# Optimization experiments

Measured on AMD Instinct MI355X. Metric: run time of the kernel, lower is better.

## Reference

```python
import jax, jax.numpy as jnp
import numpy as np

D_HID = 512
N_HEADS = 16
D_HEAD = D_HID // N_HEADS  # 32
D_FFN = 2048
B, N = 4, 1024
FACTOR = 0.5 / np.sqrt(D_HEAD)
EPS = 1e-5


def layer_norm(x, g, b):
    m = x.mean(-1, keepdims=True)
    v = ((x - m) ** 2).mean(-1, keepdims=True)
    return (x - m) / jnp.sqrt(v + EPS) * g + b


def setup_inputs() -> dict:
    key = jax.random.key(0)
    ks = jax.random.split(key, 24)
    s = 0.02
    p = lambda k, shape: jax.random.normal(k, shape, jnp.float32) * s
    inp = {
        'H': jax.random.normal(ks[0], (B, N, D_HID), jnp.float32),
        'V': jax.random.normal(ks[1], (B, N, 3, D_HID), jnp.float32),
        'D_batch': jax.random.normal(ks[2], (B, N, N), jnp.float32),
        'rbf_bias': jax.random.normal(ks[3], (B, 1, N, N), jnp.float32),
        'H_mask': jax.random.randint(ks[4], (B, N), 0, 2, jnp.int32),
        # attention sublayer params
        'g1': jnp.ones((D_HID,), jnp.float32), 'beta1': jnp.zeros((D_HID,), jnp.float32),
        'Wq': p(ks[5], (D_HID, 4 * D_HID)), 'bq': p(ks[6], (4 * D_HID,)),
        'Wk': p(ks[7], (D_HID, 4 * D_HID)), 'bk': p(ks[8], (4 * D_HID,)),
        'Wv': p(ks[9], (D_HID, D_HID)), 'bv': p(ks[10], (D_HID,)),
        'Wvv': p(ks[11], (D_HID, D_HID)),
        'Wo': p(ks[12], (D_HID, D_HID)), 'bo': p(ks[13], (D_HID,)),
        'Wvo': p(ks[14], (D_HID, D_HID)),
        # GVP FFN sublayer params
        'g2': jnp.ones((D_HID,), jnp.float32), 'beta2': jnp.zeros((D_HID,), jnp.float32),
        'Wlv': p(ks[15], (D_HID, 2 * D_HID)),
        'W1': p(ks[16], (2 * D_HID, D_FFN)), 'b1f': p(ks[17], (D_FFN,)),
        'W2': p(ks[18], (D_FFN, 2 * D_HID)), 'b2f': p(ks[19], (2 * D_HID,)),
    }
    return inp


def ept_forward(H, V, D_batch, rbf_bias, H_mask, g1, beta1, Wq, bq, Wk, bk, Wv, bv,
                Wvv, Wo, bo, Wvo, g2, beta2, Wlv, W1, b1f, W2, b2f):
    b, n, d = H.shape
    # ---- attention sublayer (pre-LN on H only, residual on H and V) ----
    Hn = layer_norm(H, g1, beta1)
    Hq = (Hn @ Wq + bq).reshape(b, n, N_HEADS, 4 * D_HEAD)
    Hk = (Hn @ Wk + bk).reshape(b, n, N_HEADS, 4 * D_HEAD)
    Hv = (Hn @ Wv + bv).reshape(b, n, N_HEADS, D_HEAD)
    # vector values: [b,n,3,d] -> [b,n,heads,3*dh]
    Vv = (V @ Wvv).reshape(b, n, 3, N_HEADS, D_HEAD).transpose(0, 1, 3, 2, 4)
    Vv = Vv.reshape(b, n, N_HEADS, 3 * D_HEAD)
    V_attn = jnp.concatenate([Hv, Vv], axis=-1)  # [b,n,h,4*dh]
    bias = rbf_bias + D_batch[:, None]  # [b,1,n,n]
    keep = (H_mask != 0)[:, None, None, :]  # mask keys
    bias = jnp.where(keep, bias, -jnp.inf)
    logits = jnp.einsum('bnhd,bmhd->bhnm', Hq, Hk) * FACTOR + bias
    attn = jax.nn.softmax(logits, axis=-1)
    res = jnp.einsum('bhnm,bmhd->bnhd', attn, V_attn)  # [b,n,h,4*dh]
    H_res = res[..., :D_HEAD].reshape(b, n, d)
    V_res = res[..., D_HEAD:].reshape(b, n, N_HEADS, 3, D_HEAD)
    V_res = V_res.transpose(0, 1, 3, 2, 4).reshape(b, n, 3, d)
    H = H + H_res @ Wo + bo
    V = V + V_res @ Wvo
    # ---- GVP FFN sublayer (pre-LN on H only, residual) ----
    Hn2 = layer_norm(H, g2, beta2)
    Vp = V @ Wlv  # [b,n,3,2d]
    V1, V2 = Vp[..., :d], Vp[..., d:]
    scaler = jnp.concatenate([Hn2, jnp.sqrt((V1 ** 2).sum(axis=-2))], axis=-1)
    h = jax.nn.silu(scaler @ W1 + b1f) @ W2 + b2f  # [b,n,2d]
    H = H + h[..., :d]
    V = V + h[..., None, d:] * V2
    return H, V


def reference(H, V, D_batch, rbf_bias, H_mask, g1, beta1, Wq, bq, Wk, bk, Wv, bv,
              Wvv, Wo, bo, Wvo, g2, beta2, Wlv, W1, b1f, W2, b2f):
    return ept_forward(H, V, D_batch, rbf_bias, H_mask, g1, beta1, Wq, bq, Wk, bk,
                       Wv, bv, Wvv, Wo, bo, Wvo, g2, beta2, Wlv, W1, b1f, W2, b2f)
```

## Files before the change

kernel.cpp:

```cpp
#include <hip/hip_runtime.h>
#include <math.h>

#define NBATCH 4
#define NSEQ   1024
#define DHID   512
#define NHEADS 16
#define ROWS   (NBATCH*NSEQ)
#define VROWS  (ROWS*3)
#define ATT_FACTOR 0.08838834764831845f
#define LOG2E 1.4426950408889634f
#define F2 (ATT_FACTOR*LOG2E)
#define SM_SHIFT (16.0f*LOG2E)

typedef __attribute__((ext_vector_type(8))) short short8;
typedef __attribute__((ext_vector_type(4))) float floatx4;

#define AS1 __attribute__((address_space(1)))
#define AS3 __attribute__((address_space(3)))
#define GLOAD_LDS16(g, l) \
  __builtin_amdgcn_global_load_lds((const AS1 void*)(g), (AS3 void*)(l), 16, 0, 0)

__device__ __forceinline__ ushort f2bf(float x) {
  union { float f; unsigned u; } v; v.f = x;
  unsigned r = v.u + 0x7fff + ((v.u >> 16) & 1);
  return (ushort)(r >> 16);
}
__device__ __forceinline__ float bf2f(ushort u) {
  union { unsigned u; float f; } v; v.u = ((unsigned)u) << 16; return v.f;
}

template<int OBF>
__global__ __launch_bounds__(256) void ln_kernel(
    const float* __restrict__ x, void* __restrict__ y, int ystride,
    const float* __restrict__ g, const float* __restrict__ beta)
{
  int row = blockIdx.x;
  int t = threadIdx.x;
  const float* xr = x + (size_t)row * DHID;
  float2 v = ((const float2*)xr)[t];
  float s  = v.x + v.y;
  float ss = v.x*v.x + v.y*v.y;
  #pragma unroll
  for (int off = 32; off > 0; off >>= 1) {
    s  += __shfl_down(s, off);
    ss += __shfl_down(ss, off);
  }
  __shared__ float red[8];
  int w = t >> 6;
  if ((t & 63) == 0) { red[w*2] = s; red[w*2+1] = ss; }
  __syncthreads();
  s  = red[0] + red[2] + red[4] + red[6];
  ss = red[1] + red[3] + red[5] + red[7];
  float mean = s * (1.0f/DHID);
  float var  = ss * (1.0f/DHID) - mean*mean;
  float rstd = rsqrtf(var + 1e-5f);
  float2 gg = ((const float2*)g)[t];
  float2 bb = ((const float2*)beta)[t];
  float2 o;
  o.x = (v.x - mean) * rstd * gg.x + bb.x;
  o.y = (v.y - mean) * rstd * gg.y + bb.y;
  if constexpr (OBF) {
    ushort2 u = { f2bf(o.x), f2bf(o.y) };
    *(ushort2*)&((ushort*)y)[(size_t)row * ystride + 2*t] = u;
  } else {
    *(float2*)&((float*)y)[(size_t)row * ystride + 2*t] = o;
  }
}

struct WJobs {
  const float* src[9];
  ushort*      dst[9];
  int K[9];
  int N[9];
  int blk0[10];
};

__global__ __launch_bounds__(256) void wtrans_all_kernel(WJobs J)
{
  __shared__ float Ts[64][65];
  int bid = blockIdx.x;
  int j = 0;
  #pragma unroll
  for (int i = 1; i < 9; i++) if (bid >= J.blk0[i]) j = i;
  const float* W = J.src[j];
  ushort* Wt = J.dst[j];
  int K = J.K[j], N = J.N[j];
  int local = bid - J.blk0[j];
  int nx = N >> 6;
  int bx = local - (local / nx) * nx;
  int by = local / nx;
  int k0 = by*64, n0 = bx*64;
  int t = threadIdx.x;
  #pragma unroll
  for (int p = 0; p < 4; p++) {
    int f = p*256 + t;
    int r = f >> 4, c = (f & 15)*4;
    float4 v = *(const float4*)&W[(size_t)(k0+r)*N + n0 + c];
    Ts[r][c] = v.x; Ts[r][c+1] = v.y; Ts[r][c+2] = v.z; Ts[r][c+3] = v.w;
  }
  __syncthreads();
  #pragma unroll
  for (int p = 0; p < 2; p++) {
    int gidx = p*256 + t;
    int nr = gidx >> 3, kc = (gidx & 7)*8;
    ushort u[8];
    #pragma unroll
    for (int x = 0; x < 8; x++) u[x] = f2bf(Ts[kc+x][nr]);
    ushort4 a = {u[0],u[1],u[2],u[3]}, b4 = {u[4],u[5],u[6],u[7]};
    *(ushort4*)&Wt[(size_t)(n0+nr)*K + k0 + kc]     = a;
    *(ushort4*)&Wt[(size_t)(n0+nr)*K + k0 + kc + 4] = b4;
  }
}

__global__ __launch_bounds__(256) void conv_bf16_kernel(
    const float* __restrict__ x, ushort* __restrict__ y)
{
  int i = blockIdx.x*256 + threadIdx.x;
  float4 v = ((const float4*)x)[i];
  ushort4 u = { f2bf(v.x), f2bf(v.y), f2bf(v.z), f2bf(v.w) };
  ((ushort4*)y)[i] = u;
}

__global__ __launch_bounds__(256) void biascat_kernel(
    const float* __restrict__ bq, const float* __restrict__ bk,
    const float* __restrict__ bv, float* __restrict__ o)
{
  int i = blockIdx.x*256 + threadIdx.x;
  float v = (i < 2048) ? bq[i] : (i < 4096 ? bk[i-2048] : bv[i-4096]);
  o[i] = v;
}

template<int ACT, int HAS_BIAS, int HAS_RES, int OUT_BF16, int DUAL>
__global__ __launch_bounds__(256) void gemm_mfma_kernel(
    const ushort* __restrict__ A, const ushort* __restrict__ Bt,
    const float* __restrict__ bias, const float* __restrict__ resid,
    void* __restrict__ Cv, ushort* __restrict__ C2,
    int M, int N, int K)
{
  __shared__ ushort As[2][128*32];
  __shared__ ushort Bs[2][128*32];
  int t = threadIdx.x;
  int w = t >> 6, lane = t & 63;
  int q16 = lane & 15, quad = lane >> 4;
  int m0 = blockIdx.y * 128, n0 = blockIdx.x * 128;
  int wm = (w & 1) * 64, wn = (w >> 1) * 64;

  int r0 = t >> 2;
  int c0 = (t & 3) * 8;
  const ushort* Ag = A  + (size_t)(m0 + r0) * K + c0;
  const ushort* Bg = Bt + (size_t)(n0 + r0) * K + c0;
  int wb = w * 512;

  floatx4 acc[4][4];
  #pragma unroll
  for (int i = 0; i < 4; i++)
    #pragma unroll
    for (int j = 0; j < 4; j++) acc[i][j] = (floatx4){0.f,0.f,0.f,0.f};

  #define STAGE(buf, kk) do { \
    GLOAD_LDS16(Ag + (kk),                 &As[buf][wb]); \
    GLOAD_LDS16(Ag + (size_t)64*K + (kk),  &As[buf][2048 + wb]); \
    GLOAD_LDS16(Bg + (kk),                 &Bs[buf][wb]); \
    GLOAD_LDS16(Bg + (size_t)64*K + (kk),  &Bs[buf][2048 + wb]); \
  } while (0)

  STAGE(0, 0);
  __syncthreads();

  int nt = K >> 5;
  int cur = 0;
  for (int kt = 0; kt < nt; kt++) {
    if (kt + 1 < nt) STAGE(cur ^ 1, (kt + 1) * 32);
    short8 af[4], bf4[4];
    #pragma unroll
    for (int i = 0; i < 4; i++) {
      af[i]  = *(const short8*)&As[cur][(wm + i*16 + q16)*32 + quad*8];
      bf4[i] = *(const short8*)&Bs[cur][(wn + i*16 + q16)*32 + quad*8];
    }
    #pragma unroll
    for (int i = 0; i < 4; i++)
      #pragma unroll
      for (int j = 0; j < 4; j++)
        acc[i][j] = __builtin_amdgcn_mfma_f32_16x16x32_bf16(af[i], bf4[j], acc[i][j], 0, 0, 0);
    __syncthreads();
    cur ^= 1;
  }
  #undef STAGE

  float* Cf = (float*)Cv;
  ushort* Cu = (ushort*)Cv;
  float bj[4];
  #pragma unroll
  for (int j = 0; j < 4; j++)
    bj[j] = HAS_BIAS ? bias[n0 + wn + j*16 + q16] : 0.f;
  #pragma unroll
  for (int i = 0; i < 4; i++) {
    #pragma unroll
    for (int r = 0; r < 4; r++) {
      int row = m0 + wm + i*16 + quad*4 + r;
      size_t base = (size_t)row * N;
      #pragma unroll
      for (int j = 0; j < 4; j++) {
        int col = n0 + wn + j*16 + q16;
        float v = acc[i][j][r] + bj[j];
        if constexpr (ACT == 1) v = v / (1.f + __expf(-v));
        if constexpr (HAS_RES) v += resid[base + col];
        if constexpr (OUT_BF16) Cu[base + col] = f2bf(v);
        else                    Cf[base + col] = v;
        if constexpr (DUAL) C2[base + col] = f2bf(v);
      }
    }
  }
}

__global__ __launch_bounds__(256) void bias2_kernel(
    const float* __restrict__ Db, const float* __restrict__ Rb,
    const int* __restrict__ Mask, ushort* __restrict__ Bc2)
{
  int i2 = blockIdx.x*256 + threadIdx.x;
  int e = i2 * 2;
  int b = e >> 20;
  int m = e & 1023;
  float2 d = *(const float2*)&Db[e];
  float2 r = *(const float2*)&Rb[e];
  ushort2 o;
  o.x = Mask[b*NSEQ + m]     ? f2bf((d.x + r.x)*LOG2E) : f2bf(-1e30f);
  o.y = Mask[b*NSEQ + m + 1] ? f2bf((d.y + r.y)*LOG2E) : f2bf(-1e30f);
  *(ushort2*)&Bc2[e] = o;
}

__global__ __launch_bounds__(256) void vtrans_kernel(
    const ushort* __restrict__ QKV, const ushort* __restrict__ VVr,
    ushort* __restrict__ Vt)
{
  __shared__ float Ts[64][33];
  int t = threadIdx.x;
  int bh = blockIdx.z;
  int b = bh >> 4, h = bh & 15;
  int dt = blockIdx.y;
  int nt = blockIdx.x;
  int d0 = dt*32, n0 = nt*64;
  #pragma unroll
  for (int i = 0; i < 2; i++) {
    int nl = (t >> 3) + i*32;
    int c4 = (t & 7)*4;
    const ushort* src;
    if (dt == 0) src = &QKV[(size_t)(b*NSEQ + n0 + nl)*4608 + 4096 + h*32 + c4];
    else { int c = dt - 1; src = &VVr[((size_t)(b*NSEQ + n0 + nl)*3 + c)*512 + h*32 + c4]; }
    ushort4 v = *(const ushort4*)src;
    Ts[nl][c4] = bf2f(v.x); Ts[nl][c4+1] = bf2f(v.y);
    Ts[nl][c4+2] = bf2f(v.z); Ts[nl][c4+3] = bf2f(v.w);
  }
  __syncthreads();
  int dl = t >> 3;
  int n8 = (t & 7)*8;
  ushort u[8];
  #pragma unroll
  for (int k = 0; k < 8; k++) u[k] = f2bf(Ts[n8+k][dl]);
  size_t ob = ((size_t)bh*128 + d0 + dl)*NSEQ + n0 + n8;
  ushort4 u0 = {u[0],u[1],u[2],u[3]}, u1 = {u[4],u[5],u[6],u[7]};
  *(ushort4*)&Vt[ob]     = u0;
  *(ushort4*)&Vt[ob + 4] = u1;
}

__global__ __launch_bounds__(256) void attn_mfma_kernel(
    const ushort* __restrict__ QKV,
    const ushort* __restrict__ Vt, const ushort* __restrict__ Bc2,
    ushort* __restrict__ HRES, ushort* __restrict__ VRES)
{
  __shared__ union {
    ushort q[64][136];
    struct { ushort k[32][136]; ushort v[128][40]; } kv;
  } S;
  __shared__ ushort Ps[4][16][40];

  int t = threadIdx.x;
  int w = t >> 6, lane = t & 63;
  int q16 = lane & 15, quad = lane >> 4;
  int h = blockIdx.x, qt = blockIdx.y, b = blockIdx.z;
  int q0 = qt * 64;

  #pragma unroll
  for (int i = 0; i < 4; i++) {
    int f = t + i*256;
    int r = f >> 4, c8 = f & 15;
    *(float4*)&S.q[r][c8*8] =
        *(const float4*)&QKV[(size_t)(b*NSEQ + q0 + r)*4608 + h*128 + c8*8];
  }
  __syncthreads();
  short8 qf[4];
  #pragma unroll
  for (int c = 0; c < 4; c++)
    qf[c] = *(const short8*)&S.q[w*16 + q16][c*32 + quad*8];

  floatx4 o[8];
  #pragma unroll
  for (int i = 0; i < 8; i++) o[i] = (floatx4){0.f,0.f,0.f,0.f};
  float l_i[4] = {0.f,0.f,0.f,0.f};
  const ushort* bias_base = Bc2 + (size_t)(b*NSEQ + q0 + w*16)*NSEQ;

  for (int m0 = 0; m0 < NSEQ; m0 += 32) {
    __syncthreads();
    #pragma unroll
    for (int i = 0; i < 2; i++) {
      int f = t + i*256;
      int r = f >> 4, c8 = f & 15;
      *(float4*)&S.kv.k[r][c8*8] =
          *(const float4*)&QKV[(size_t)(b*NSEQ + m0 + r)*4608 + 2048 + h*128 + c8*8];
    }
    #pragma unroll
    for (int i = 0; i < 2; i++) {
      int f = t + i*256;
      int d = f >> 2, g = f & 3;
      *(float4*)&S.kv.v[d][g*8] =
          *(const float4*)&Vt[((size_t)(b*NHEADS + h)*128 + d)*NSEQ + m0 + g*8];
    }
    __syncthreads();

    floatx4 s0 = (floatx4){0.f,0.f,0.f,0.f};
    floatx4 s1 = (floatx4){0.f,0.f,0.f,0.f};
    #pragma unroll
    for (int c = 0; c < 4; c++) {
      short8 k0 = *(const short8*)&S.kv.k[q16][c*32 + quad*8];
      short8 k1 = *(const short8*)&S.kv.k[q16 + 16][c*32 + quad*8];
      s0 = __builtin_amdgcn_mfma_f32_16x16x32_bf16(qf[c], k0, s0, 0, 0, 0);
      s1 = __builtin_amdgcn_mfma_f32_16x16x32_bf16(qf[c], k1, s1, 0, 0, 0);
    }
    #pragma unroll
    for (int i = 0; i < 4; i++) {
      int row = quad*4 + i;
      const ushort* bp = bias_base + (size_t)row*NSEQ + m0 + q16;
      float v0 = s0[i]*F2 + bf2f(bp[0]);
      float v1 = s1[i]*F2 + bf2f(bp[16]);
      float p0 = exp2f(v0 - SM_SHIFT);
      float p1 = exp2f(v1 - SM_SHIFT);
      Ps[w][row][q16]      = f2bf(p0);
      Ps[w][row][16 + q16] = f2bf(p1);
      l_i[i] += p0 + p1;
    }
    short8 pf = *(const short8*)&Ps[w][q16][quad*8];
    #pragma unroll
    for (int tt = 0; tt < 8; tt++) {
      short8 vf = *(const short8*)&S.kv.v[tt*16 + q16][quad*8];
      o[tt] = __builtin_amdgcn_mfma_f32_16x16x32_bf16(pf, vf, o[tt], 0, 0, 0);
    }
  }
  #pragma unroll
  for (int i = 0; i < 4; i++) {
    float l = l_i[i];
    l += __shfl_xor(l, 1); l += __shfl_xor(l, 2);
    l += __shfl_xor(l, 4); l += __shfl_xor(l, 8);
    float inv = 1.0f / l;
    int grow = b*NSEQ + q0 + w*16 + quad*4 + i;
    #pragma unroll
    for (int tt = 0; tt < 2; tt++)
      HRES[(size_t)grow*512 + h*32 + tt*16 + q16] = f2bf(o[tt][i] * inv);
    #pragma unroll
    for (int tt = 2; tt < 8; tt++) {
      int c = (tt - 2) >> 1;
      int jj = ((tt - 2) & 1)*16 + q16;
      VRES[((size_t)grow*3 + c)*512 + h*32 + jj] = f2bf(o[tt][i] * inv);
    }
  }
}

__global__ __launch_bounds__(256) void vnorm_kernel(
    const float* __restrict__ VP, ushort* __restrict__ SC)
{
  int idx = blockIdx.x*256 + threadIdx.x;
  int row = idx >> 9;
  int d = idx & 511;
  const float* p = VP + (size_t)row*3072 + d;
  float a = p[0], b = p[1024], c = p[2048];
  SC[(size_t)row*1024 + 512 + d] = f2bf(sqrtf(a*a + b*b + c*c));
}

__global__ __launch_bounds__(256) void finale_kernel(
    const float* __restrict__ HH, const float* __restrict__ VP,
    float* __restrict__ Hout, float* __restrict__ Vout)
{
  int idx = blockIdx.x*256 + threadIdx.x;
  if (idx < ROWS*DHID) {
    int row = idx >> 9;
    int d = idx & 511;
    Hout[idx] += HH[(size_t)row*1024 + d];
  } else {
    int k = idx - ROWS*DHID;
    int r3 = k >> 9;
    int d = k & 511;
    int row = r3 / 3;
    Vout[k] += HH[(size_t)row*1024 + 512 + d] * VP[(size_t)r3*1024 + 512 + d];
  }
}

extern "C" void kernel_launch(void* const* d_in, const int* in_sizes, int n_in,
                              void* d_out, int out_size, void* d_ws, size_t ws_size,
                              hipStream_t stream)
{
  const float* H    = (const float*)d_in[0];
  const float* V    = (const float*)d_in[1];
  const float* Db   = (const float*)d_in[2];
  const float* Rb   = (const float*)d_in[3];
  const int*   Mask = (const int*)d_in[4];
  const float* g1   = (const float*)d_in[5];
  const float* be1  = (const float*)d_in[6];
  const float* Wq   = (const float*)d_in[7];
  const float* bq   = (const float*)d_in[8];
  const float* Wk   = (const float*)d_in[9];
  const float* bkk  = (const float*)d_in[10];
  const float* Wv   = (const float*)d_in[11];
  const float* bv   = (const float*)d_in[12];
  const float* Wvv  = (const float*)d_in[13];
  const float* Wo   = (const float*)d_in[14];
  const float* bo   = (const float*)d_in[15];
  const float* Wvo  = (const float*)d_in[16];
  const float* g2   = (const float*)d_in[17];
  const float* be2  = (const float*)d_in[18];
  const float* Wlv  = (const float*)d_in[19];
  const float* W1   = (const float*)d_in[20];
  const float* b1f  = (const float*)d_in[21];
  const float* W2   = (const float*)d_in[22];
  const float* b2f  = (const float*)d_in[23];

  float* Hout = (float*)d_out;
  float* Vout = Hout + (size_t)ROWS*DHID;

  char* w = (char*)d_ws;
  const size_t MB = 1024*1024;
  const size_t KB = 1024;
  ushort* WqT  = (ushort*)(w + 0);
  ushort* WkT  = (ushort*)(w + 2048*KB);
  ushort* WvT  = (ushort*)(w + 4096*KB);
  ushort* WvvT = (ushort*)(w + 4608*KB);
  ushort* WoT  = (ushort*)(w + 5120*KB);
  ushort* WvoT = (ushort*)(w + 5632*KB);
  ushort* WlvT = (ushort*)(w + 6144*KB);
  ushort* W1T  = (ushort*)(w + 7168*KB);
  ushort* W2T  = (ushort*)(w + 11264*KB);
  float*  Bqkv = (float*)(w + 15360*KB);
  ushort* HNbf  = (ushort*)(w + 16*MB);
  ushort* QKVbf = (ushort*)(w + 20*MB);
  ushort* VVrbf = (ushort*)(w + 56*MB);
  ushort* Vbf   = (ushort*)(w + 68*MB);
  ushort* Vtb   = (ushort*)(w + 80*MB);
  ushort* Bc2   = (ushort*)(w + 96*MB);
  ushort* HRESbf = (ushort*)(w + 104*MB);
  ushort* VRESbf = (ushort*)(w + 108*MB);
  ushort* Voutbf = (ushort*)(w + 20*MB);
  float*  VP     = (float*)(w + 56*MB);
  ushort* SCbf   = (ushort*)(w + 104*MB);
  ushort* S1bf   = (ushort*)(w + 112*MB);
  float*  HHb    = (float*)(w + 32*MB);

  dim3 blk(256);

  WJobs J;
  const float* ws_[9] = {Wq, Wk, Wv, Wvv, Wo, Wvo, Wlv, W1, W2};
  ushort* wd_[9] = {WqT, WkT, WvT, WvvT, WoT, WvoT, WlvT, W1T, W2T};
  int wk_[9] = {512, 512, 512, 512, 512, 512, 512, 1024, 2048};
  int wn_[9] = {2048, 2048, 512, 512, 512, 512, 1024, 2048, 1024};
  int off = 0;
  for (int i = 0; i < 9; i++) {
    J.src[i] = ws_[i]; J.dst[i] = wd_[i]; J.K[i] = wk_[i]; J.N[i] = wn_[i];
    J.blk0[i] = off;
    off += (wn_[i] >> 6) * (wk_[i] >> 6);
  }
  J.blk0[9] = off;
  wtrans_all_kernel<<<off, blk, 0, stream>>>(J);

  ln_kernel<1><<<ROWS, blk, 0, stream>>>(H, HNbf, DHID, g1, be1);
  conv_bf16_kernel<<<(VROWS*DHID/4)/256, blk, 0, stream>>>(V, Vbf);
  biascat_kernel<<<18, blk, 0, stream>>>(bq, bkk, bv, Bqkv);

  gemm_mfma_kernel<0,1,0,1,0><<<dim3(36, 32), blk, 0, stream>>>(HNbf, WqT, Bqkv, nullptr, QKVbf, nullptr, 4096, 4608, 512);
  gemm_mfma_kernel<0,0,0,1,0><<<dim3( 4, 96), blk, 0, stream>>>(Vbf, WvvT, nullptr, nullptr, VVrbf, nullptr, 12288, 512, 512);

  bias2_kernel<<<(NBATCH*NSEQ*NSEQ/2)/256, blk, 0, stream>>>(Db, Rb, Mask, Bc2);
  vtrans_kernel<<<dim3(16, 4, 64), blk, 0, stream>>>(QKVbf, VVrbf, Vtb);

  attn_mfma_kernel<<<dim3(16, 16, 4), blk, 0, stream>>>(QKVbf, Vtb, Bc2, HRESbf, VRESbf);

  gemm_mfma_kernel<0,1,1,0,0><<<dim3(4, 32), blk, 0, stream>>>(HRESbf, WoT,  bo, H, Hout, nullptr, 4096, 512, 512);
  gemm_mfma_kernel<0,0,1,0,1><<<dim3(4, 96), blk, 0, stream>>>(VRESbf, WvoT, nullptr, V, Vout, Voutbf, 12288, 512, 512);

  ln_kernel<1><<<ROWS, blk, 0, stream>>>(Hout, SCbf, 1024, g2, be2);
  gemm_mfma_kernel<0,0,0,0,0><<<dim3(8, 96), blk, 0, stream>>>(Voutbf, WlvT, nullptr, nullptr, VP, nullptr, 12288, 1024, 512);
  vnorm_kernel<<<(ROWS*DHID)/256, blk, 0, stream>>>(VP, SCbf);

  gemm_mfma_kernel<1,1,0,1,0><<<dim3(16, 32), blk, 0, stream>>>(SCbf, W1T, b1f, nullptr, S1bf, nullptr, 4096, 2048, 1024);
  gemm_mfma_kernel<0,1,0,0,0><<<dim3( 8, 32), blk, 0, stream>>>(S1bf, W2T, b2f, nullptr, HHb, nullptr, 4096, 1024, 2048);

  finale_kernel<<<((ROWS + VROWS)*DHID)/256, blk, 0, stream>>>(HHb, VP, Hout, Vout);
}
```

Baseline: 493.7 us.

## Enlarge attention tiles and prefetch K/V/bias tiles through registers

The attention kernel now processes 128 query rows per block (32 per wave) and 64 keys per iteration. K, V and bias tiles for the next step are prefetched into registers while the current tile is computed, and the bias is staged through shared memory instead of being read per-lane from global. This amortizes K/V loads over more queries, coalesces the bias reads and hides global latency, with s_setprio around the MFMA bursts. In exchange it uses more registers and LDS and launches half as many blocks, which lowers parallelism.

```diff
diff --git a/kernel.cpp b/kernel.cpp
--- a/kernel.cpp
+++ b/kernel.cpp
@@ -263,103 +263,157 @@
   *(ushort4*)&Vt[ob + 4] = u1;
 }
 
-__global__ __launch_bounds__(256) void attn_mfma_kernel(
+__global__ __launch_bounds__(256, 2) void attn_mfma_kernel(
     const ushort* __restrict__ QKV,
     const ushort* __restrict__ Vt, const ushort* __restrict__ Bc2,
     ushort* __restrict__ HRES, ushort* __restrict__ VRES)
 {
   __shared__ union {
-    ushort q[64][136];
-    struct { ushort k[32][136]; ushort v[128][40]; } kv;
+    ushort q[128][136];
+    struct {
+      ushort k[64][136];
+      ushort v[128][72];
+      ushort bias[128][72];
+    } s;
   } S;
-  __shared__ ushort Ps[4][16][40];
+  __shared__ ushort Ps[4][32][72];
 
   int t = threadIdx.x;
   int w = t >> 6, lane = t & 63;
   int q16 = lane & 15, quad = lane >> 4;
   int h = blockIdx.x, qt = blockIdx.y, b = blockIdx.z;
-  int q0 = qt * 64;
-
-  #pragma unroll
-  for (int i = 0; i < 4; i++) {
+  int q0 = qt * 128;
+
+  float4 rk[4], rv[4], rb[4];
+  const size_t kbase = (size_t)(b*NSEQ)*4608 + 2048 + h*128 + (t&3)*8;
+  const size_t vbase = ((size_t)(b*NHEADS + h)*128 + (t>>3))*NSEQ + (t&7)*8;
+  const size_t bbase = (size_t)(b*NSEQ + q0 + (t>>3))*NSEQ + (t&7)*8;
+  int kr = t >> 2;
+
+  #define LOADT(m0_) do { \
+    _Pragma("unroll") \
+    for (int u = 0; u < 4; u++) { \
+      rk[u] = *(const float4*)&QKV[kbase + (size_t)((m0_) + kr)*4608 + u*32]; \
+      rv[u] = *(const float4*)&Vt[vbase + (size_t)u*32*NSEQ + (m0_)]; \
+      rb[u] = *(const float4*)&Bc2[bbase + (size_t)u*32*NSEQ + (m0_)]; \
+    } \
+  } while (0)
+
+  #define STORET() do { \
+    _Pragma("unroll") \
+    for (int u = 0; u < 4; u++) { \
+      *(float4*)&S.s.k[kr][(t&3)*8 + u*32]       = rk[u]; \
+      *(float4*)&S.s.v[(t>>3) + u*32][(t&7)*8]   = rv[u]; \
+      *(float4*)&S.s.bias[(t>>3) + u*32][(t&7)*8] = rb[u]; \
+    } \
+  } while (0)
+
+  LOADT(0);
+
+  #pragma unroll
+  for (int i = 0; i < 8; i++) {
     int f = t + i*256;
     int r = f >> 4, c8 = f & 15;
     *(float4*)&S.q[r][c8*8] =
         *(const float4*)&QKV[(size_t)(b*NSEQ + q0 + r)*4608 + h*128 + c8*8];
   }
   __syncthreads();
-  short8 qf[4];
-  #pragma unroll
-  for (int c = 0; c < 4; c++)
-    qf[c] = *(const short8*)&S.q[w*16 + q16][c*32 + quad*8];
-
-  floatx4 o[8];
-  #pragma unroll
-  for (int i = 0; i < 8; i++) o[i] = (floatx4){0.f,0.f,0.f,0.f};
-  float l_i[4] = {0.f,0.f,0.f,0.f};
-  const ushort* bias_base = Bc2 + (size_t)(b*NSEQ + q0 + w*16)*NSEQ;
-
-  for (int m0 = 0; m0 < NSEQ; m0 += 32) {
+  short8 qf[2][4];
+  #pragma unroll
+  for (int rg = 0; rg < 2; rg++)
+    #pragma unroll
+    for (int c = 0; c < 4; c++)
+      qf[rg][c] = *(const short8*)&S.q[w*32 + rg*16 + q16][c*32 + quad*8];
+
+  floatx4 o[2][8];
+  #pragma unroll
+  for (int rg = 0; rg < 2; rg++)
+    #pragma unroll
+    for (int i = 0; i < 8; i++) o[rg][i] = (floatx4){0.f,0.f,0.f,0.f};
+  float l_i[2][4] = {{0.f,0.f,0.f,0.f},{0.f,0.f,0.f,0.f}};
+
+  #pragma unroll 1
+  for (int it = 0; it < 16; it++) {
     __syncthreads();
-    #pragma unroll
-    for (int i = 0; i < 2; i++) {
-      int f = t + i*256;
-      int r = f >> 4, c8 = f & 15;
-      *(float4*)&S.kv.k[r][c8*8] =
-          *(const float4*)&QKV[(size_t)(b*NSEQ + m0 + r)*4608 + 2048 + h*128 + c8*8];
+    STORET();
+    if (it < 15) LOADT((it + 1) * 64);
+    __syncthreads();
+
+    floatx4 sf[2][4];
+    #pragma unroll
+    for (int rg = 0; rg < 2; rg++)
+      #pragma unroll
+      for (int g = 0; g < 4; g++) sf[rg][g] = (floatx4){0.f,0.f,0.f,0.f};
+    __builtin_amdgcn_s_setprio(1);
+    #pragma unroll
+    for (int c = 0; c < 4; c++) {
+      short8 kf[4];
+      #pragma unroll
+      for (int g = 0; g < 4; g++)
+        kf[g] = *(const short8*)&S.s.k[g*16 + q16][c*32 + quad*8];
+      #pragma unroll
+      for (int rg = 0; rg < 2; rg++)
+        #pragma unroll
+        for (int g = 0; g < 4; g++)
+          sf[rg][g] = __builtin_amdgcn_mfma_f32_16x16x32_bf16(qf[rg][c], kf[g], sf[rg][g], 0, 0, 0);
     }
-    #pragma unroll
-    for (int i = 0; i < 2; i++) {
-      int f = t + i*256;
-      int d = f >> 2, g = f & 3;
-      *(float4*)&S.kv.v[d][g*8] =
-          *(const float4*)&Vt[((size_t)(b*NHEADS + h)*128 + d)*NSEQ + m0 + g*8];
+    __builtin_amdgcn_s_setprio(0);
+
+    #pragma unroll
+    for (int rg = 0; rg < 2; rg++) {
+      #pragma unroll
+      for (int i = 0; i < 4; i++) {
+        int row = w*32 + rg*16 + quad*4 + i;
+        #pragma unroll
+        for (int g = 0; g < 4; g++) {
+          float v = sf[rg][g][i]*F2 + bf2f(S.s.bias[row][g*16 + q16]);
+          float p = exp2f(v - SM_SHIFT);
+          Ps[w][rg*16 + quad*4 + i][g*16 + q16] = f2bf(p);
+          l_i[rg][i] += p;
+        }
+      }
     }
-    __syncthreads();
-
-    floatx4 s0 = (floatx4){0.f,0.f,0.f,0.f};
-    floatx4 s1 = (floatx4){0.f,0.f,0.f,0.f};
-    #pragma unroll
-    for (int c = 0; c < 4; c++) {
-      short8 k0 = *(const short8*)&S.kv.k[q16][c*32 + quad*8];
-      short8 k1 = *(const short8*)&S.kv.k[q16 + 16][c*32 + quad*8];
-      s0 = __builtin_amdgcn_mfma_f32_16x16x32_bf16(qf[c], k0, s0, 0, 0, 0);
-      s1 = __builtin_amdgcn_mfma_f32_16x16x32_bf16(qf[c], k1, s1, 0, 0, 0);
+
+    short8 pf[2][2];
+    #pragma unroll
+    for (int rg = 0; rg < 2; rg++)
+      #pragma unroll
+      for (int ks = 0; ks < 2; ks++)
+        pf[rg][ks] = *(const short8*)&Ps[w][rg*16 + q16][ks*32 + quad*8];
+    __builtin_amdgcn_s_setprio(1);
+    #pragma unroll
+    for (int tt = 0; tt < 8; tt++) {
+      short8 vf0 = *(const short8*)&S.s.v[tt*16 + q16][quad*8];
+      short8 vf1 = *(const short8*)&S.s.v[tt*16 + q16][32 + quad*8];
+      #pragma unroll
+      for (int rg = 0; rg < 2; rg++) {
+        o[rg][tt] = __builtin_amdgcn_mfma_f32_16x16x32_bf16(pf[rg][0], vf0, o[rg][tt], 0, 0, 0);
+        o[rg][tt] = __builtin_amdgcn_mfma_f32_16x16x32_bf16(pf[rg][1], vf1, o[rg][tt], 0, 0, 0);
+      }
     }
+    __builtin_amdgcn_s_setprio(0);
+  }
+  #undef LOADT
+  #undef STORET
+
+  #pragma unroll
+  for (int rg = 0; rg < 2; rg++) {
     #pragma unroll
     for (int i = 0; i < 4; i++) {
-      int row = quad*4 + i;
-      const ushort* bp = bias_base + (size_t)row*NSEQ + m0 + q16;
-      float v0 = s0[i]*F2 + bf2f(bp[0]);
-      float v1 = s1[i]*F2 + bf2f(bp[16]);
-      float p0 = exp2f(v0 - SM_SHIFT);
-      float p1 = exp2f(v1 - SM_SHIFT);
-      Ps[w][row][q16]      = f2bf(p0);
-      Ps[w][row][16 + q16] = f2bf(p1);
-      l_i[i] += p0 + p1;
-    }
-    short8 pf = *(const short8*)&Ps[w][q16][quad*8];
-    #pragma unroll
-    for (int tt = 0; tt < 8; tt++) {
-      short8 vf = *(const short8*)&S.kv.v[tt*16 + q16][quad*8];
-      o[tt] = __builtin_amdgcn_mfma_f32_16x16x32_bf16(pf, vf, o[tt], 0, 0, 0);
-    }
-  }
-  #pragma unroll
-  for (int i = 0; i < 4; i++) {
-    float l = l_i[i];
-    l += __shfl_xor(l, 1); l += __shfl_xor(l, 2);
-    l += __shfl_xor(l, 4); l += __shfl_xor(l, 8);
-    float inv = 1.0f / l;
-    int grow = b*NSEQ + q0 + w*16 + quad*4 + i;
-    #pragma unroll
-    for (int tt = 0; tt < 2; tt++)
-      HRES[(size_t)grow*512 + h*32 + tt*16 + q16] = f2bf(o[tt][i] * inv);
-    #pragma unroll
-    for (int tt = 2; tt < 8; tt++) {
-      int c = (tt - 2) >> 1;
-      int jj = ((tt - 2) & 1)*16 + q16;
-      VRES[((size_t)grow*3 + c)*512 + h*32 + jj] = f2bf(o[tt][i] * inv);
+      float l = l_i[rg][i];
+      l += __shfl_xor(l, 1); l += __shfl_xor(l, 2);
+      l += __shfl_xor(l, 4); l += __shfl_xor(l, 8);
+      float inv = 1.0f / l;
+      int grow = b*NSEQ + q0 + w*32 + rg*16 + quad*4 + i;
+      #pragma unroll
+      for (int tt = 0; tt < 2; tt++)
+        HRES[(size_t)grow*512 + h*32 + tt*16 + q16] = f2bf(o[rg][tt][i] * inv);
+      #pragma unroll
+      for (int tt = 2; tt < 8; tt++) {
+        int c = (tt - 2) >> 1;
+        int jj = ((tt - 2) & 1)*16 + q16;
+        VRES[((size_t)grow*3 + c)*512 + h*32 + jj] = f2bf(o[rg][tt][i] * inv);
+      }
     }
   }
 }
@@ -478,7 +532,7 @@
   bias2_kernel<<<(NBATCH*NSEQ*NSEQ/2)/256, blk, 0, stream>>>(Db, Rb, Mask, Bc2);
   vtrans_kernel<<<dim3(16, 4, 64), blk, 0, stream>>>(QKVbf, VVrbf, Vtb);
 
-  attn_mfma_kernel<<<dim3(16, 16, 4), blk, 0, stream>>>(QKVbf, Vtb, Bc2, HRESbf, VRESbf);
+  attn_mfma_kernel<<<dim3(16, 8, 4), blk, 0, stream>>>(QKVbf, Vtb, Bc2, HRESbf, VRESbf);
 
   gemm_mfma_kernel<0,1,1,0,0><<<dim3(4, 32), blk, 0, stream>>>(HRESbf, WoT,  bo, H, Hout, nullptr, 4096, 512, 512);
   gemm_mfma_kernel<0,0,1,0,1><<<dim3(4, 96), blk, 0, stream>>>(VRESbf, WvoT, nullptr, V, Vout, Voutbf, 12288, 512, 512);
```

After: 566.1 us. 14.7% more time.
